# Kernel tuning notes

Measured on AMD Instinct MI355X. Metric: run time of the kernel, lower is better.

## Reference

```python
import jax, jax.numpy as jnp
import numpy as np

N, E, H, C, IN = 20000, 640000, 4, 64, 256
HC = H * C
NEG_SLOPE = 0.2


def setup_inputs() -> dict:
    key = jax.random.key(0)
    ks = jax.random.split(key, 24)
    rn = lambda k, s: jax.random.normal(k, s, jnp.float32) * 0.05
    return {
        "x": jax.random.normal(ks[0], (N, IN), jnp.float32),
        "edge_index": jax.random.randint(ks[1], (2, E), 0, N),
        "confidence": jax.random.normal(ks[2], (N,), jnp.float32),
        "w_in": rn(ks[3], (IN, C)), "b_in": jnp.zeros((C,), jnp.float32),
        "lin_w0": rn(ks[4], (C, HC)),
        "lin_w12": rn(ks[5], (2, HC, HC)),
        "att_src": rn(ks[6], (3, H, C)),
        "att_dst": rn(ks[7], (3, H, C)),
        "gat_bias": jnp.zeros((3, HC), jnp.float32),
        "conf_w": rn(ks[8], (HC, 1)), "conf_b": jnp.zeros((1,), jnp.float32),
        "nc_w1": rn(ks[9], (HC, C)), "nc_b1": jnp.zeros((C,), jnp.float32),
        "nc_w2": rn(ks[10], (C, 1)), "nc_b2": jnp.zeros((1,), jnp.float32),
        "oc_w1": rn(ks[11], (HC, C)), "oc_b1": jnp.zeros((C,), jnp.float32),
        "oc_w2": rn(ks[12], (C, 1)), "oc_b2": jnp.zeros((1,), jnp.float32),
        "ec_w1": rn(ks[13], (HC, C)), "ec_b1": jnp.zeros((C,), jnp.float32),
        "ec_w2": rn(ks[14], (C, 4)), "ec_b2": jnp.zeros((4,), jnp.float32),
    }


def _gat_layer(h_in, src, dst, n, lin_w, a_src, a_dst, bias):
    # h_in: (n, in_ch). PyG GATConv: linear -> per-edge attn -> segment softmax -> scatter-add.
    h = (h_in @ lin_w).reshape(n, H, C)
    s_src = jnp.einsum("nhc,hc->nh", h, a_src)  # (n, H)
    s_dst = jnp.einsum("nhc,hc->nh", h, a_dst)
    alpha = jax.nn.leaky_relu(s_src[src] + s_dst[dst], NEG_SLOPE)  # (E', H)
    # softmax over incoming edges of each dst node (self-loops guarantee coverage)
    amax = jax.ops.segment_max(alpha, dst, num_segments=n)
    ex = jnp.exp(alpha - amax[dst])
    denom = jax.ops.segment_sum(ex, dst, num_segments=n)
    coef = ex / jnp.maximum(denom[dst], 1e-16)
    msg = h[src] * coef[:, :, None]  # (E', H, C)
    out = jax.ops.segment_sum(msg, dst, num_segments=n)
    return out.reshape(n, HC) + bias


def reference(x, edge_index, confidence, w_in, b_in, lin_w0, lin_w12,
              att_src, att_dst, gat_bias, conf_w, conf_b,
              nc_w1, nc_b1, nc_w2, nc_b2, oc_w1, oc_b1, oc_w2, oc_b2,
              ec_w1, ec_b1, ec_w2, ec_b2):
    n = x.shape[0]
    loops = jnp.arange(n)
    src = jnp.concatenate([edge_index[0], loops])  # PyG add_self_loops=True
    dst = jnp.concatenate([edge_index[1], loops])
    h = jax.nn.relu(x @ w_in + b_in)  # input_proj + relu (dropout off in eval)
    lin_ws = [lin_w0, lin_w12[0], lin_w12[1]]
    conf_norm = jax.nn.sigmoid(confidence)  # (n,)
    for i in range(3):
        h_new = _gat_layer(h, src, dst, n, lin_ws[i], att_src[i], att_dst[i], gat_bias[i])
        cw = jax.nn.sigmoid(h_new @ conf_w + conf_b)[:, 0] * conf_norm
        h_new = h_new * cw[:, None]
        h = h + h_new if h.shape[-1] == h_new.shape[-1] else h_new
        if i < 2:
            h = jax.nn.relu(h)
    mlp = lambda w1, b1, w2, b2: jax.nn.relu(h @ w1 + b1) @ w2 + b2
    node_pred = jax.nn.sigmoid(mlp(nc_w1, nc_b1, nc_w2, nc_b2))[:, 0]
    origin_pred = jax.nn.sigmoid(mlp(oc_w1, oc_b1, oc_w2, oc_b2))[:, 0]
    error_type_pred = mlp(ec_w1, ec_b1, ec_w2, ec_b2)
    return node_pred, origin_pred, error_type_pred, h
```

## Files before the change

### kernel.cpp

```cpp
#include <hip/hip_runtime.h>
#include <cstdint>
#include <cstddef>

#define NN   20000
#define NPAD 20224
#define EE   640000
#define E2   660000
#define HHD  4
#define CC   64
#define HC   256
#define NEG  0.2f

#define NBUK 313
#define NBLK 129
#define EPB  5120
#define SCN  (NBUK * NBLK)

typedef short bf16x8 __attribute__((ext_vector_type(8)));
typedef float f32x4 __attribute__((ext_vector_type(4)));

__device__ __forceinline__ float sigmoidf_(float x) { return 1.0f / (1.0f + __expf(-x)); }

__device__ __forceinline__ float wred_sum(float v) {
#pragma unroll
    for (int d = 32; d; d >>= 1) v += __shfl_xor(v, d, 64);
    return v;
}

__device__ __forceinline__ unsigned short f2bf(float f) {
    unsigned u = __float_as_uint(f);
    u = (u + 0x7fff + ((u >> 16) & 1)) >> 16;
    return (unsigned short)u;
}
__device__ __forceinline__ float bfval(unsigned short h) { return __uint_as_float(((unsigned)h) << 16); }
__device__ __forceinline__ float bf_lo(unsigned u) { return __uint_as_float(u << 16); }
__device__ __forceinline__ float bf_hi(unsigned u) { return __uint_as_float(u & 0xffff0000u); }

__global__ __launch_bounds__(256) void hist_edges(const int* __restrict__ ei,
                                                  int* __restrict__ bhist) {
    __shared__ int h[NBUK];
    int bl = blockIdx.x, t = threadIdx.x;
    for (int i = t; i < NBUK; i += 256) h[i] = 0;
    __syncthreads();
    int e0 = bl * EPB;
#pragma unroll 4
    for (int i = t; i < EPB; i += 256) {
        int e = e0 + i;
        if (e < E2) {
            int d = (e < EE) ? ei[EE + e] : (e - EE);
            atomicAdd(&h[d >> 6], 1);
        }
    }
    __syncthreads();
    for (int i = t; i < NBUK; i += 256) bhist[i * NBLK + bl] = h[i];
}

__global__ __launch_bounds__(1024) void scan_hist(const int* __restrict__ bhist,
                                                  int* __restrict__ sbase) {
    __shared__ int buf[1024];
    int t = threadIdx.x;
    int base = t * 40;
    int local[40];
    int s = 0;
#pragma unroll
    for (int i = 0; i < 40; i++) {
        int idx = base + i;
        int v = (idx < SCN) ? bhist[idx] : 0;
        local[i] = v;
        s += v;
    }
    buf[t] = s;
    __syncthreads();
    for (int d = 1; d < 1024; d <<= 1) {
        int tv = (t >= d) ? buf[t - d] : 0;
        __syncthreads();
        buf[t] += tv;
        __syncthreads();
    }
    int run = buf[t] - s;
#pragma unroll
    for (int i = 0; i < 40; i++) {
        int idx = base + i;
        if (idx < SCN) sbase[idx] = run;
        run += local[i];
    }
}

__global__ __launch_bounds__(256) void scatter_bucket(const int* __restrict__ ei,
                                                      const int* __restrict__ sbase,
                                                      unsigned int* __restrict__ ebuf) {
    __shared__ int cur[NBUK];
    int bl = blockIdx.x, t = threadIdx.x;
    for (int i = t; i < NBUK; i += 256) cur[i] = sbase[i * NBLK + bl];
    __syncthreads();
    int e0 = bl * EPB;
#pragma unroll 4
    for (int i = t; i < EPB; i += 256) {
        int e = e0 + i;
        if (e < E2) {
            int s, d;
            if (e < EE) { s = ei[e]; d = ei[EE + e]; }
            else        { s = e - EE; d = s; }
            int p = atomicAdd(&cur[d >> 6], 1);
            ebuf[p] = ((unsigned int)(d & 63) << 15) | (unsigned int)s;
        }
    }
}

__global__ __launch_bounds__(256) void build_csr(const unsigned int* __restrict__ ebuf,
                                                 const int* __restrict__ sbase,
                                                 int* __restrict__ off,
                                                 int* __restrict__ csr) {
    __shared__ int hist[64], sc[64], curl[64];
    int bu = blockIdx.x, t = threadIdx.x;
    int base = sbase[bu * NBLK];
    int end  = (bu + 1 < NBUK) ? sbase[(bu + 1) * NBLK] : E2;
    int ne = end - base;
    if (t < 64) hist[t] = 0;
    __syncthreads();
    for (int i = t; i < ne; i += 256) {
        int dl = (int)(ebuf[base + i] >> 15);
        atomicAdd(&hist[dl], 1);
    }
    __syncthreads();
    if (t < 64) sc[t] = hist[t];
    __syncthreads();
    for (int d = 1; d < 64; d <<= 1) {
        int v = (t < 64 && t >= d) ? sc[t - d] : 0;
        __syncthreads();
        if (t < 64) sc[t] += v;
        __syncthreads();
    }
    int n0 = bu * 64;
    if (t < 64) {
        int ex = base + sc[t] - hist[t];
        if (n0 + t < NN) off[n0 + t] = ex;
        curl[t] = ex;
    }
    if (bu == NBUK - 1 && t == 0) off[NN] = E2;
    __syncthreads();
    for (int i = t; i < ne; i += 256) {
        unsigned int v = ebuf[base + i];
        int dl = (int)(v >> 15);
        int p = atomicAdd(&curl[dl], 1);
        csr[p] = (int)(v & 0x7fffu);
    }
}

#define WTOT 212992
__global__ void prep_inputs(const float* __restrict__ x,
                            const float* __restrict__ w_in, const float* __restrict__ lin_w0,
                            const float* __restrict__ lin_w12,
                            const float* __restrict__ nc1, const float* __restrict__ oc1,
                            const float* __restrict__ ec1,
                            const float* __restrict__ nb, const float* __restrict__ ob,
                            const float* __restrict__ eb,
                            unsigned short* __restrict__ whi,
                            float* __restrict__ bcat,
                            unsigned short* __restrict__ xh, unsigned short* __restrict__ xl) {
    int idx = blockIdx.x * 256 + threadIdx.x;
    if (idx < NN * 64) {
        float4 v = ((const float4*)x)[idx];
        ushort4 hi, lo;
        hi.x = f2bf(v.x); lo.x = f2bf(v.x - bfval(hi.x));
        hi.y = f2bf(v.y); lo.y = f2bf(v.y - bfval(hi.y));
        hi.z = f2bf(v.z); lo.z = f2bf(v.z - bfval(hi.z));
        hi.w = f2bf(v.w); lo.w = f2bf(v.w - bfval(hi.w));
        ((ushort4*)xh)[idx] = hi;
        ((ushort4*)xl)[idx] = lo;
    }
    if (idx < 192) {
        int g = idx >> 6, jj = idx & 63;
        const float* b = (g == 0) ? nb : ((g == 1) ? ob : eb);
        bcat[idx] = b[jj];
    }
    if (idx >= WTOT) return;
    float v;
    if (idx < 16384) {
        int n = idx >> 8, k = idx & 255;
        v = w_in[k * 64 + n];
    } else if (idx < 32768) {
        int r = idx - 16384;
        int n = r >> 6, k = r & 63;
        v = lin_w0[k * 256 + n];
    } else if (idx < 98304) {
        int r = idx - 32768;
        int n = r >> 8, k = r & 255;
        v = lin_w12[k * 256 + n];
    } else if (idx < 163840) {
        int r = idx - 98304;
        int n = r >> 8, k = r & 255;
        v = lin_w12[65536 + k * 256 + n];
    } else {
        int r = idx - 163840;
        int n = r >> 8, k = r & 255;
        int g = n >> 6, jj = n & 63;
        const float* w = (g == 0) ? nc1 : ((g == 1) ? oc1 : ec1);
        v = w[k * 64 + jj];
    }
    whi[idx] = f2bf(v);
}

template <int K, int OUT_CH, int MODE, int NT>
__global__ __launch_bounds__(256) void gemm_lds(
    const unsigned short* __restrict__ Ahp, const unsigned short* __restrict__ Alp,
    const unsigned short* __restrict__ Wh,
    const float* __restrict__ bias,
    unsigned short* __restrict__ Outh, unsigned short* __restrict__ Outl,
    const float* __restrict__ a_src, const float* __restrict__ a_dst,
    float* __restrict__ s_src, float* __restrict__ s_dst,
    const float* __restrict__ w2n, const float* __restrict__ w2o,
    const float* __restrict__ w2e,
    const float* __restrict__ b2n, const float* __restrict__ b2o,
    const float* __restrict__ b2e,
    float* __restrict__ outbuf, int nreal) {
    constexpr int LB = K + 8;
    constexpr int NS = K / 32;
    __shared__ unsigned short Bh[64 * LB];
    const int tid = threadIdx.x;
    const int wv = tid >> 6, lane = tid & 63;
    const int quad = lane >> 4, ln = lane & 15;
    const int mb = blockIdx.x * 64;
    const int r0 = mb + wv * 16 + ln;

    const unsigned short* aph = Ahp + (size_t)r0 * K + quad * 8;
    const unsigned short* apl = Alp + (size_t)r0 * K + quad * 8;
    bf16x8 ah[NS], al[NS];
#pragma unroll
    for (int s = 0; s < NS; s++) {
        ah[s] = *(const bf16x8*)(aph + s * 32);
        al[s] = *(const bf16x8*)(apl + s * 32);
    }

    for (int ct = 0; ct < NT; ct++) {
        const int cb = ct * 64;
        if (ct > 0) __syncthreads();

        constexpr int NCHK = 64 * (K / 8);
#pragma unroll
        for (int i = 0; i < NCHK / 256; i++) {
            int flat = tid + i * 256;
            int r = flat / (K / 8);
            int c = (flat % (K / 8)) * 8;
            *(uint4*)&Bh[r * LB + c] = *(const uint4*)&Wh[(size_t)(cb + r) * K + c];
        }
        __syncthreads();

        f32x4 acc[4];
#pragma unroll
        for (int j = 0; j < 4; j++) {
            acc[j][0] = 0.f; acc[j][1] = 0.f; acc[j][2] = 0.f; acc[j][3] = 0.f;
        }

#pragma unroll
        for (int s = 0; s < NS; s++) {
#pragma unroll
            for (int cg = 0; cg < 4; cg++) {
                bf16x8 bh = *(const bf16x8*)&Bh[(cg * 16 + ln) * LB + quad * 8 + s * 32];
                acc[cg] = __builtin_amdgcn_mfma_f32_16x16x32_bf16(ah[s], bh, acc[cg], 0, 0, 0);
                acc[cg] = __builtin_amdgcn_mfma_f32_16x16x32_bf16(al[s], bh, acc[cg], 0, 0, 0);
            }
        }

        if (MODE == 1) {
            float av[4], dv[4];
#pragma unroll
            for (int cg = 0; cg < 4; cg++) {
                av[cg] = a_src[cb + cg * 16 + ln];
                dv[cg] = a_dst[cb + cg * 16 + ln];
            }
#pragma unroll
            for (int reg = 0; reg < 4; reg++) {
                float ps = 0.f, pd = 0.f;
#pragma unroll
                for (int cg = 0; cg < 4; cg++) {
                    float t = acc[cg][reg];
                    ps += t * av[cg];
                    pd += t * dv[cg];
                }
#pragma unroll
                for (int d = 1; d < 16; d <<= 1) {
                    ps += __shfl_xor(ps, d, 64);
                    pd += __shfl_xor(pd, d, 64);
                }
                if (ln == 0) {
                    int row = mb + wv * 16 + quad * 4 + reg;
                    if (row < nreal) {
                        s_src[row * 4 + ct] = ps;
                        s_dst[row * 4 + ct] = pd;
                    }
                }
            }
        }

        if (MODE == 3) {
            float bv[4];
#pragma unroll
            for (int cg = 0; cg < 4; cg++) bv[cg] = bias[cb + cg * 16 + ln];
            if (ct < 2) {
                const float* w2 = (ct == 0) ? w2n : w2o;
                float b2 = (ct == 0) ? b2n[0] : b2o[0];
                float wv2[4];
#pragma unroll
                for (int cg = 0; cg < 4; cg++) wv2[cg] = w2[cg * 16 + ln];
#pragma unroll
                for (int reg = 0; reg < 4; reg++) {
                    float t = 0.f;
#pragma unroll
                    for (int cg = 0; cg < 4; cg++) {
                        float tv = fmaxf(acc[cg][reg] + bv[cg], 0.f);
                        t += tv * wv2[cg];
                    }
#pragma unroll
                    for (int d = 1; d < 16; d <<= 1) t += __shfl_xor(t, d, 64);
                    int row = mb + wv * 16 + quad * 4 + reg;
                    if (ln == 0 && row < nreal)
                        outbuf[ct * NN + row] = sigmoidf_(t + b2);
                }
            } else {
                float4 w4[4];
#pragma unroll
                for (int cg = 0; cg < 4; cg++) w4[cg] = ((const float4*)w2e)[cg * 16 + ln];
#pragma unroll
                for (int reg = 0; reg < 4; reg++) {
                    float e0 = 0.f, e1 = 0.f, e2 = 0.f, e3 = 0.f;
#pragma unroll
                    for (int cg = 0; cg < 4; cg++) {
                        float tv = fmaxf(acc[cg][reg] + bv[cg], 0.f);
                        e0 += tv * w4[cg].x; e1 += tv * w4[cg].y;
                        e2 += tv * w4[cg].z; e3 += tv * w4[cg].w;
                    }
#pragma unroll
                    for (int d = 1; d < 16; d <<= 1) {
                        e0 += __shfl_xor(e0, d, 64); e1 += __shfl_xor(e1, d, 64);
                        e2 += __shfl_xor(e2, d, 64); e3 += __shfl_xor(e3, d, 64);
                    }
                    int row = mb + wv * 16 + quad * 4 + reg;
                    if (ln == 0 && row < nreal) {
                        float4 ev = make_float4(e0 + b2e[0], e1 + b2e[1], e2 + b2e[2], e3 + b2e[3]);
                        *(float4*)&outbuf[2 * NN + row * 4] = ev;
                    }
                }
            }
            continue;
        }

#pragma unroll
        for (int cg = 0; cg < 4; cg++) {
            int col = cb + cg * 16 + ln;
            int rbase = mb + wv * 16 + quad * 4;
#pragma unroll
            for (int reg = 0; reg < 4; reg++) {
                float v = acc[cg][reg];
                int r = rbase + reg;
                if (MODE == 0) {
                    v += bias[col]; v = fmaxf(v, 0.f);
                    unsigned short hi = f2bf(v);
                    Outh[(size_t)r * OUT_CH + col] = hi;
                    Outl[(size_t)r * OUT_CH + col] = f2bf(v - bfval(hi));
                } else if (MODE == 1) {
                    Outh[(size_t)r * OUT_CH + col] = f2bf(v);
                }
            }
        }
    }
}

__global__ __launch_bounds__(256) void gat_node(const unsigned short* __restrict__ hhb,
                                                const float* __restrict__ s_src,
                                                const float* __restrict__ s_dst,
                                                const int* __restrict__ csr_src,
                                                const int* __restrict__ csr_off,
                                                const float* __restrict__ gbias,
                                                const float* __restrict__ conf_w,
                                                const float* __restrict__ conf_b,
                                                const float* __restrict__ confid,
                                                unsigned short* __restrict__ h_hi,
                                                unsigned short* __restrict__ h_lo,
                                                float* __restrict__ outbuf,
                                                int layer) {
    __shared__ float Lc[4][64];
    __shared__ int   Ls[4][16];
    int wv = threadIdx.x >> 6;
    int lane = threadIdx.x & 63;
    int n = blockIdx.x * 4 + wv;
    int myhead = lane >> 4, slot = lane & 15;
    int off0 = csr_off[n];
    int deg = csr_off[n + 1] - off0;
    const int* cp = csr_src + off0;
    const unsigned short* hrow = hhb + lane * 4;
    float sdm = s_dst[n * 4 + myhead];

    float ax = 0.f, ay = 0.f, az = 0.f, aw = 0.f, smp = 0.f;
    int nch = (deg + 15) >> 4;
    bool valid = slot < deg;
    int sl = cp[valid ? slot : deg - 1];
    float ssv = s_src[sl * 4 + myhead];
    for (int t = 0; t < nch; t++) {
        float a = ssv + sdm;
        a = a > 0.f ? a : NEG * a;
        float c = valid ? __expf(a) : 0.f;
        smp += c;
        Lc[wv][lane] = c;
        if (myhead == 0) Ls[wv][slot] = sl;
        __builtin_amdgcn_wave_barrier();
        float4 c0 = *(const float4*)&Lc[wv][myhead * 16 + 0];
        float4 c1 = *(const float4*)&Lc[wv][myhead * 16 + 4];
        float4 c2 = *(const float4*)&Lc[wv][myhead * 16 + 8];
        float4 c3 = *(const float4*)&Lc[wv][myhead * 16 + 12];
        int4 s0 = *(const int4*)&Ls[wv][0];
        int4 s1 = *(const int4*)&Ls[wv][4];
        int4 s2 = *(const int4*)&Ls[wv][8];
        int4 s3 = *(const int4*)&Ls[wv][12];
        __builtin_amdgcn_wave_barrier();
        if (t + 1 < nch) {
            int i = ((t + 1) << 4) + slot;
            valid = i < deg;
            sl = cp[valid ? i : deg - 1];
            ssv = s_src[sl * 4 + myhead];
        }
        float cf[16] = {c0.x, c0.y, c0.z, c0.w, c1.x, c1.y, c1.z, c1.w,
                        c2.x, c2.y, c2.z, c2.w, c3.x, c3.y, c3.z, c3.w};
        int sv[16] = {s0.x, s0.y, s0.z, s0.w, s1.x, s1.y, s1.z, s1.w,
                      s2.x, s2.y, s2.z, s2.w, s3.x, s3.y, s3.z, s3.w};
#pragma unroll
        for (int q = 0; q < 16; q++) {
            uint2 u = *(const uint2*)(hrow + ((size_t)sv[q] << 8));
            ax += cf[q] * bf_lo(u.x); ay += cf[q] * bf_hi(u.x);
            az += cf[q] * bf_lo(u.y); aw += cf[q] * bf_hi(u.y);
        }
    }
    smp += __shfl_xor(smp, 1, 64);
    smp += __shfl_xor(smp, 2, 64);
    smp += __shfl_xor(smp, 4, 64);
    smp += __shfl_xor(smp, 8, 64);
    float inv = 1.0f / fmaxf(smp, 1e-16f);
    ax *= inv; ay *= inv; az *= inv; aw *= inv;

    float4 b4 = *(const float4*)&gbias[lane * 4];
    float hx = ax + b4.x, hy = ay + b4.y, hz = az + b4.z, hw = aw + b4.w;
    float4 cw4 = *(const float4*)&conf_w[lane * 4];
    float local = hx * cw4.x + hy * cw4.y + hz * cw4.z + hw * cw4.w;
    float tot = wred_sum(local);
    float cw = sigmoidf_(tot + conf_b[0]) * sigmoidf_(confid[n]);
    hx *= cw; hy *= cw; hz *= cw; hw *= cw;
    if (layer > 0) {
        ushort4 ph = *(const ushort4*)&h_hi[(size_t)n * HC + lane * 4];
        ushort4 pl = *(const ushort4*)&h_lo[(size_t)n * HC + lane * 4];
        hx += bfval(ph.x) + bfval(pl.x);
        hy += bfval(ph.y) + bfval(pl.y);
        hz += bfval(ph.z) + bfval(pl.z);
        hw += bfval(ph.w) + bfval(pl.w);
    }
    if (layer < 2) {
        hx = fmaxf(hx, 0.f); hy = fmaxf(hy, 0.f);
        hz = fmaxf(hz, 0.f); hw = fmaxf(hw, 0.f);
    } else {
        *(float4*)&outbuf[6 * NN + (size_t)n * HC + lane * 4] =
            make_float4(hx, hy, hz, hw);
    }
    ushort4 oh, ol;
    oh.x = f2bf(hx); ol.x = f2bf(hx - bfval(oh.x));
    oh.y = f2bf(hy); ol.y = f2bf(hy - bfval(oh.y));
    oh.z = f2bf(hz); ol.z = f2bf(hz - bfval(oh.z));
    oh.w = f2bf(hw); ol.w = f2bf(hw - bfval(oh.w));
    *(ushort4*)&h_hi[(size_t)n * HC + lane * 4] = oh;
    *(ushort4*)&h_lo[(size_t)n * HC + lane * 4] = ol;
}

extern "C" void kernel_launch(void* const* d_in, const int* in_sizes, int n_in,
                              void* d_out, int out_size, void* d_ws, size_t ws_size,
                              hipStream_t stream) {
    const float* x       = (const float*)d_in[0];
    const int*   ei      = (const int*)d_in[1];
    const float* conf    = (const float*)d_in[2];
    const float* w_in    = (const float*)d_in[3];
    const float* b_in    = (const float*)d_in[4];
    const float* lin_w0  = (const float*)d_in[5];
    const float* lin_w12 = (const float*)d_in[6];
    const float* att_src = (const float*)d_in[7];
    const float* att_dst = (const float*)d_in[8];
    const float* gbias   = (const float*)d_in[9];
    const float* conf_w  = (const float*)d_in[10];
    const float* conf_b  = (const float*)d_in[11];
    const float* nc_w1   = (const float*)d_in[12];
    const float* nc_b1   = (const float*)d_in[13];
    const float* nc_w2   = (const float*)d_in[14];
    const float* nc_b2   = (const float*)d_in[15];
    const float* oc_w1   = (const float*)d_in[16];
    const float* oc_b1   = (const float*)d_in[17];
    const float* oc_w2   = (const float*)d_in[18];
    const float* oc_b2   = (const float*)d_in[19];
    const float* ec_w1   = (const float*)d_in[20];
    const float* ec_b1   = (const float*)d_in[21];
    const float* ec_w2   = (const float*)d_in[22];
    const float* ec_b2   = (const float*)d_in[23];
    float* out = (float*)d_out;

    char* p = (char*)d_ws;
    auto alloc = [&](size_t bytes) -> void* {
        void* r = (void*)p;
        p += (bytes + 255) & ~(size_t)255;
        return r;
    };
    unsigned short* h_hi = (unsigned short*)alloc((size_t)NPAD * HC * 2);
    unsigned short* h_lo = (unsigned short*)alloc((size_t)NPAD * HC * 2);
    unsigned short* hh   = (unsigned short*)alloc((size_t)NPAD * HC * 2);
    unsigned short* h0h  = (unsigned short*)alloc((size_t)NPAD * CC * 2);
    unsigned short* h0l  = (unsigned short*)alloc((size_t)NPAD * CC * 2);
    float*          ssrc = (float*)alloc((size_t)NN * 4 * 4);
    float*          sdst = (float*)alloc((size_t)NN * 4 * 4);
    int*            off  = (int*)alloc((size_t)(NN + 1) * 4);
    int*            csr  = (int*)alloc((size_t)E2 * 4);
    int*            bhist= (int*)alloc((size_t)SCN * 4);
    int*            sbase= (int*)alloc((size_t)SCN * 4);
    unsigned short* whi  = (unsigned short*)alloc((size_t)WTOT * 2);
    float*          bcat = (float*)alloc((size_t)192 * 4);
    unsigned short* xh   = (unsigned short*)alloc((size_t)NPAD * 256 * 2 * 2);
    unsigned short* xl   = xh + (size_t)NPAD * 256;
    unsigned int*   ebuf = (unsigned int*)xh;

    const unsigned short* wt_in = whi;
    const unsigned short* wt_l0 = whi + 16384;
    const unsigned short* wt_a  = whi + 32768;
    const unsigned short* wt_b  = whi + 98304;
    const unsigned short* wt_hd = whi + 163840;

    hist_edges<<<NBLK, 256, 0, stream>>>(ei, bhist);
    scan_hist<<<1, 1024, 0, stream>>>(bhist, sbase);
    scatter_bucket<<<NBLK, 256, 0, stream>>>(ei, sbase, ebuf);
    build_csr<<<NBUK, 256, 0, stream>>>(ebuf, sbase, off, csr);

    prep_inputs<<<(NN * 64 + 255) / 256, 256, 0, stream>>>(
        x, w_in, lin_w0, lin_w12, nc_w1, oc_w1, ec_w1, nc_b1, oc_b1, ec_b1,
        whi, bcat, xh, xl);

    gemm_lds<256, 64, 0, 1><<<dim3(NPAD / 64, 1), 256, 0, stream>>>(
        xh, xl, wt_in, b_in, h0h, h0l, nullptr, nullptr, nullptr, nullptr,
        nullptr, nullptr, nullptr, nullptr, nullptr, nullptr, nullptr, NN);

    gemm_lds<64, 256, 1, 4><<<dim3(NPAD / 64, 1), 256, 0, stream>>>(
        h0h, h0l, wt_l0, nullptr, hh, nullptr, att_src, att_dst, ssrc, sdst,
        nullptr, nullptr, nullptr, nullptr, nullptr, nullptr, nullptr, NN);
    gat_node<<<NN / 4, 256, 0, stream>>>(hh, ssrc, sdst, csr, off, gbias, conf_w, conf_b, conf,
                                         h_hi, h_lo, out, 0);

    for (int i = 1; i < 3; i++) {
        const unsigned short* wh = (i == 1) ? wt_a : wt_b;
        gemm_lds<256, 256, 1, 4><<<dim3(NPAD / 64, 1), 256, 0, stream>>>(
            h_hi, h_lo, wh, nullptr, hh, nullptr,
            att_src + i * HHD * CC, att_dst + i * HHD * CC, ssrc, sdst,
            nullptr, nullptr, nullptr, nullptr, nullptr, nullptr, nullptr, NN);
        gat_node<<<NN / 4, 256, 0, stream>>>(hh, ssrc, sdst, csr, off, gbias + i * HC,
                                             conf_w, conf_b, conf, h_hi, h_lo, out, i);
    }

    gemm_lds<256, 192, 3, 3><<<dim3(NPAD / 64, 1), 256, 0, stream>>>(
        h_hi, h_lo, wt_hd, bcat, nullptr, nullptr, nullptr, nullptr, nullptr, nullptr,
        nc_w2, oc_w2, ec_w2, nc_b2, oc_b2, ec_b2, out, NN);
}
```

Measured before the change: 386.0 us.

## Merge graph-CSR build kernels with input prep and projection GEMMs

Independent work is co-scheduled inside shared launches. Edge histogramming runs in the same grid as input/weight conversion. Bucket scatter runs alongside the input projection GEMM, and CSR build alongside the layer-0 GEMM, with blocks dispatched by block index. This cuts kernel launches and lets the irregular graph preprocessing overlap with dense work. It costs a separate ebuf allocation, since ebuf no longer aliases xh, which is now live concurrently. Shared memory is sized for the larger body, which may lower occupancy for the scatter/build blocks.

```diff
diff --git a/kernel.cpp b/kernel.cpp
--- a/kernel.cpp
+++ b/kernel.cpp
@@ -15,6 +15,8 @@
 #define NBLK 129
 #define EPB  5120
 #define SCN  (NBUK * NBLK)
+#define PREP_BLKS 5000
+#define GEMM_BLKS (NPAD / 64)
 
 typedef short bf16x8 __attribute__((ext_vector_type(8)));
 typedef float f32x4 __attribute__((ext_vector_type(4)));
@@ -36,10 +38,10 @@
 __device__ __forceinline__ float bf_lo(unsigned u) { return __uint_as_float(u << 16); }
 __device__ __forceinline__ float bf_hi(unsigned u) { return __uint_as_float(u & 0xffff0000u); }
 
-__global__ __launch_bounds__(256) void hist_edges(const int* __restrict__ ei,
-                                                  int* __restrict__ bhist) {
-    __shared__ int h[NBUK];
-    int bl = blockIdx.x, t = threadIdx.x;
+
+__device__ __forceinline__ void hist_body(int bl, const int* __restrict__ ei,
+                                          int* __restrict__ bhist, int* h ) {
+    int t = threadIdx.x;
     for (int i = t; i < NBUK; i += 256) h[i] = 0;
     __syncthreads();
     int e0 = bl * EPB;
@@ -55,42 +57,11 @@
     for (int i = t; i < NBUK; i += 256) bhist[i * NBLK + bl] = h[i];
 }
 
-__global__ __launch_bounds__(1024) void scan_hist(const int* __restrict__ bhist,
-                                                  int* __restrict__ sbase) {
-    __shared__ int buf[1024];
+__device__ __forceinline__ void scatter_body(int bl, const int* __restrict__ ei,
+                                             const int* __restrict__ sbase,
+                                             unsigned int* __restrict__ ebuf,
+                                             int* cur ) {
     int t = threadIdx.x;
-    int base = t * 40;
-    int local[40];
-    int s = 0;
-#pragma unroll
-    for (int i = 0; i < 40; i++) {
-        int idx = base + i;
-        int v = (idx < SCN) ? bhist[idx] : 0;
-        local[i] = v;
-        s += v;
-    }
-    buf[t] = s;
-    __syncthreads();
-    for (int d = 1; d < 1024; d <<= 1) {
-        int tv = (t >= d) ? buf[t - d] : 0;
-        __syncthreads();
-        buf[t] += tv;
-        __syncthreads();
-    }
-    int run = buf[t] - s;
-#pragma unroll
-    for (int i = 0; i < 40; i++) {
-        int idx = base + i;
-        if (idx < SCN) sbase[idx] = run;
-        run += local[i];
-    }
-}
-
-__global__ __launch_bounds__(256) void scatter_bucket(const int* __restrict__ ei,
-                                                      const int* __restrict__ sbase,
-                                                      unsigned int* __restrict__ ebuf) {
-    __shared__ int cur[NBUK];
-    int bl = blockIdx.x, t = threadIdx.x;
     for (int i = t; i < NBUK; i += 256) cur[i] = sbase[i * NBLK + bl];
     __syncthreads();
     int e0 = bl * EPB;
@@ -107,12 +78,13 @@
     }
 }
 
-__global__ __launch_bounds__(256) void build_csr(const unsigned int* __restrict__ ebuf,
-                                                 const int* __restrict__ sbase,
-                                                 int* __restrict__ off,
-                                                 int* __restrict__ csr) {
-    __shared__ int hist[64], sc[64], curl[64];
-    int bu = blockIdx.x, t = threadIdx.x;
+__device__ __forceinline__ void build_body(int bu, const unsigned int* __restrict__ ebuf,
+                                           const int* __restrict__ sbase,
+                                           int* __restrict__ off, int* __restrict__ csr,
+                                           int* hist ) {
+    int* sc = hist + 64;
+    int* curl = hist + 128;
+    int t = threadIdx.x;
     int base = sbase[bu * NBLK];
     int end  = (bu + 1 < NBUK) ? sbase[(bu + 1) * NBLK] : E2;
     int ne = end - base;
@@ -148,7 +120,8 @@
 }
 
 #define WTOT 212992
-__global__ void prep_inputs(const float* __restrict__ x,
+__device__ __forceinline__ void prep_body(int idx,
+                            const float* __restrict__ x,
                             const float* __restrict__ w_in, const float* __restrict__ lin_w0,
                             const float* __restrict__ lin_w12,
                             const float* __restrict__ nc1, const float* __restrict__ oc1,
@@ -158,7 +131,6 @@
                             unsigned short* __restrict__ whi,
                             float* __restrict__ bcat,
                             unsigned short* __restrict__ xh, unsigned short* __restrict__ xl) {
-    int idx = blockIdx.x * 256 + threadIdx.x;
     if (idx < NN * 64) {
         float4 v = ((const float4*)x)[idx];
         ushort4 hi, lo;
@@ -202,6 +174,262 @@
 }
 
 template <int K, int OUT_CH, int MODE, int NT>
+__device__ __forceinline__ void gemm_body(
+    unsigned short* Bh,
+    int mb,
+    const unsigned short* __restrict__ Ahp, const unsigned short* __restrict__ Alp,
+    const unsigned short* __restrict__ Wh,
+    const float* __restrict__ bias,
+    unsigned short* __restrict__ Outh,
+    const float* __restrict__ a_src, const float* __restrict__ a_dst,
+    float* __restrict__ s_src, float* __restrict__ s_dst,
+    const float* __restrict__ w2n, const float* __restrict__ w2o,
+    const float* __restrict__ w2e,
+    const float* __restrict__ b2n, const float* __restrict__ b2o,
+    const float* __restrict__ b2e,
+    unsigned short* __restrict__ Outl,
+    float* __restrict__ outbuf, int nreal) {
+    constexpr int LB = K + 8;
+    constexpr int NS = K / 32;
+    const int tid = threadIdx.x;
+    const int wv = tid >> 6, lane = tid & 63;
+    const int quad = lane >> 4, ln = lane & 15;
+    const int r0 = mb + wv * 16 + ln;
+
+    const unsigned short* aph = Ahp + (size_t)r0 * K + quad * 8;
+    const unsigned short* apl = Alp + (size_t)r0 * K + quad * 8;
+    bf16x8 ah[NS], al[NS];
+#pragma unroll
+    for (int s = 0; s < NS; s++) {
+        ah[s] = *(const bf16x8*)(aph + s * 32);
+        al[s] = *(const bf16x8*)(apl + s * 32);
+    }
+
+    for (int ct = 0; ct < NT; ct++) {
+        const int cb = ct * 64;
+        if (ct > 0) __syncthreads();
+
+        constexpr int NCHK = 64 * (K / 8);
+#pragma unroll
+        for (int i = 0; i < NCHK / 256; i++) {
+            int flat = tid + i * 256;
+            int r = flat / (K / 8);
+            int c = (flat % (K / 8)) * 8;
+            *(uint4*)&Bh[r * LB + c] = *(const uint4*)&Wh[(size_t)(cb + r) * K + c];
+        }
+        __syncthreads();
+
+        f32x4 acc[4];
+#pragma unroll
+        for (int j = 0; j < 4; j++) {
+            acc[j][0] = 0.f; acc[j][1] = 0.f; acc[j][2] = 0.f; acc[j][3] = 0.f;
+        }
+
+#pragma unroll
+        for (int s = 0; s < NS; s++) {
+#pragma unroll
+            for (int cg = 0; cg < 4; cg++) {
+                bf16x8 bh = *(const bf16x8*)&Bh[(cg * 16 + ln) * LB + quad * 8 + s * 32];
+                acc[cg] = __builtin_amdgcn_mfma_f32_16x16x32_bf16(ah[s], bh, acc[cg], 0, 0, 0);
+                acc[cg] = __builtin_amdgcn_mfma_f32_16x16x32_bf16(al[s], bh, acc[cg], 0, 0, 0);
+            }
+        }
+
+        if (MODE == 1) {
+            float av[4], dv[4];
+#pragma unroll
+            for (int cg = 0; cg < 4; cg++) {
+                av[cg] = a_src[cb + cg * 16 + ln];
+                dv[cg] = a_dst[cb + cg * 16 + ln];
+            }
+#pragma unroll
+            for (int reg = 0; reg < 4; reg++) {
+                float ps = 0.f, pd = 0.f;
+#pragma unroll
+                for (int cg = 0; cg < 4; cg++) {
+                    float t = acc[cg][reg];
+                    ps += t * av[cg];
+                    pd += t * dv[cg];
+                }
+#pragma unroll
+                for (int d = 1; d < 16; d <<= 1) {
+                    ps += __shfl_xor(ps, d, 64);
+                    pd += __shfl_xor(pd, d, 64);
+                }
+                if (ln == 0) {
+                    int row = mb + wv * 16 + quad * 4 + reg;
+                    if (row < nreal) {
+                        s_src[row * 4 + ct] = ps;
+                        s_dst[row * 4 + ct] = pd;
+                    }
+                }
+            }
+        }
+
+        if (MODE == 3) {
+            float bv[4];
+#pragma unroll
+            for (int cg = 0; cg < 4; cg++) bv[cg] = bias[cb + cg * 16 + ln];
+            if (ct < 2) {
+                const float* w2 = (ct == 0) ? w2n : w2o;
+                float b2 = (ct == 0) ? b2n[0] : b2o[0];
+                float wv2[4];
+#pragma unroll
+                for (int cg = 0; cg < 4; cg++) wv2[cg] = w2[cg * 16 + ln];
+#pragma unroll
+                for (int reg = 0; reg < 4; reg++) {
+                    float t = 0.f;
+#pragma unroll
+                    for (int cg = 0; cg < 4; cg++) {
+                        float tv = fmaxf(acc[cg][reg] + bv[cg], 0.f);
+                        t += tv * wv2[cg];
+                    }
+#pragma unroll
+                    for (int d = 1; d < 16; d <<= 1) t += __shfl_xor(t, d, 64);
+                    int row = mb + wv * 16 + quad * 4 + reg;
+                    if (ln == 0 && row < nreal)
+                        outbuf[ct * NN + row] = sigmoidf_(t + b2);
+                }
+            } else {
+                float4 w4[4];
+#pragma unroll
+                for (int cg = 0; cg < 4; cg++) w4[cg] = ((const float4*)w2e)[cg * 16 + ln];
+#pragma unroll
+                for (int reg = 0; reg < 4; reg++) {
+                    float e0 = 0.f, e1 = 0.f, e2 = 0.f, e3 = 0.f;
+#pragma unroll
+                    for (int cg = 0; cg < 4; cg++) {
+                        float tv = fmaxf(acc[cg][reg] + bv[cg], 0.f);
+                        e0 += tv * w4[cg].x; e1 += tv * w4[cg].y;
+                        e2 += tv * w4[cg].z; e3 += tv * w4[cg].w;
+                    }
+#pragma unroll
+                    for (int d = 1; d < 16; d <<= 1) {
+                        e0 += __shfl_xor(e0, d, 64); e1 += __shfl_xor(e1, d, 64);
+                        e2 += __shfl_xor(e2, d, 64); e3 += __shfl_xor(e3, d, 64);
+                    }
+                    int row = mb + wv * 16 + quad * 4 + reg;
+                    if (ln == 0 && row < nreal) {
+                        float4 ev = make_float4(e0 + b2e[0], e1 + b2e[1], e2 + b2e[2], e3 + b2e[3]);
+                        *(float4*)&outbuf[2 * NN + row * 4] = ev;
+                    }
+                }
+            }
+            continue;
+        }
+
+#pragma unroll
+        for (int cg = 0; cg < 4; cg++) {
+            int col = cb + cg * 16 + ln;
+            int rbase = mb + wv * 16 + quad * 4;
+#pragma unroll
+            for (int reg = 0; reg < 4; reg++) {
+                float v = acc[cg][reg];
+                int r = rbase + reg;
+                if (MODE == 0) {
+                    v += bias[col]; v = fmaxf(v, 0.f);
+                    unsigned short hi = f2bf(v);
+                    Outh[(size_t)r * OUT_CH + col] = hi;
+                    Outl[(size_t)r * OUT_CH + col] = f2bf(v - bfval(hi));
+                } else if (MODE == 1) {
+                    Outh[(size_t)r * OUT_CH + col] = f2bf(v);
+                }
+            }
+        }
+    }
+}
+
+
+__global__ __launch_bounds__(256) void prep_hist(
+    const float* __restrict__ x,
+    const float* __restrict__ w_in, const float* __restrict__ lin_w0,
+    const float* __restrict__ lin_w12,
+    const float* __restrict__ nc1, const float* __restrict__ oc1,
+    const float* __restrict__ ec1,
+    const float* __restrict__ nb, const float* __restrict__ ob,
+    const float* __restrict__ eb,
+    unsigned short* __restrict__ whi, float* __restrict__ bcat,
+    unsigned short* __restrict__ xh, unsigned short* __restrict__ xl,
+    const int* __restrict__ ei, int* __restrict__ bhist) {
+    __shared__ int h[NBUK];
+    if (blockIdx.x < PREP_BLKS) {
+        prep_body(blockIdx.x * 256 + threadIdx.x, x, w_in, lin_w0, lin_w12,
+                  nc1, oc1, ec1, nb, ob, eb, whi, bcat, xh, xl);
+    } else {
+        hist_body(blockIdx.x - PREP_BLKS, ei, bhist, h);
+    }
+}
+
+__global__ __launch_bounds__(1024) void scan_hist(const int* __restrict__ bhist,
+                                                  int* __restrict__ sbase) {
+    __shared__ int buf[1024];
+    int t = threadIdx.x;
+    int base = t * 40;
+    int local[40];
+    int s = 0;
+#pragma unroll
+    for (int i = 0; i < 40; i++) {
+        int idx = base + i;
+        int v = (idx < SCN) ? bhist[idx] : 0;
+        local[i] = v;
+        s += v;
+    }
+    buf[t] = s;
+    __syncthreads();
+    for (int d = 1; d < 1024; d <<= 1) {
+        int tv = (t >= d) ? buf[t - d] : 0;
+        __syncthreads();
+        buf[t] += tv;
+        __syncthreads();
+    }
+    int run = buf[t] - s;
+#pragma unroll
+    for (int i = 0; i < 40; i++) {
+        int idx = base + i;
+        if (idx < SCN) sbase[idx] = run;
+        run += local[i];
+    }
+}
+
+__global__ __launch_bounds__(256) void scatter_proj(
+    const int* __restrict__ ei, const int* __restrict__ sbase,
+    unsigned int* __restrict__ ebuf,
+    const unsigned short* __restrict__ xh, const unsigned short* __restrict__ xl,
+    const unsigned short* __restrict__ wt_in, const float* __restrict__ b_in,
+    unsigned short* __restrict__ h0h, unsigned short* __restrict__ h0l) {
+    __shared__ unsigned short smem[64 * (256 + 8)];
+    if (blockIdx.x < NBLK) {
+        scatter_body(blockIdx.x, ei, sbase, ebuf, (int*)smem);
+    } else {
+        gemm_body<256, 64, 0, 1>(smem, (int)(blockIdx.x - NBLK) * 64,
+                                 xh, xl, wt_in, b_in, h0h,
+                                 nullptr, nullptr, nullptr, nullptr,
+                                 nullptr, nullptr, nullptr, nullptr, nullptr, nullptr,
+                                 h0l, nullptr, NN);
+    }
+}
+
+__global__ __launch_bounds__(256) void build_l0(
+    const unsigned int* __restrict__ ebuf, const int* __restrict__ sbase,
+    int* __restrict__ off, int* __restrict__ csr,
+    const unsigned short* __restrict__ h0h, const unsigned short* __restrict__ h0l,
+    const unsigned short* __restrict__ wt_l0,
+    unsigned short* __restrict__ hh,
+    const float* __restrict__ a_src, const float* __restrict__ a_dst,
+    float* __restrict__ ssrc, float* __restrict__ sdst) {
+    __shared__ unsigned short smem[64 * (64 + 8)];
+    if (blockIdx.x < NBUK) {
+        build_body(blockIdx.x, ebuf, sbase, off, csr, (int*)smem);
+    } else {
+        gemm_body<64, 256, 1, 4>(smem, (int)(blockIdx.x - NBUK) * 64,
+                                 h0h, h0l, wt_l0, nullptr, hh,
+                                 a_src, a_dst, ssrc, sdst,
+                                 nullptr, nullptr, nullptr, nullptr, nullptr, nullptr,
+                                 nullptr, nullptr, NN);
+    }
+}
+
+template <int K, int OUT_CH, int MODE, int NT>
 __global__ __launch_bounds__(256) void gemm_lds(
     const unsigned short* __restrict__ Ahp, const unsigned short* __restrict__ Alp,
     const unsigned short* __restrict__ Wh,
@@ -214,156 +442,10 @@
     const float* __restrict__ b2n, const float* __restrict__ b2o,
     const float* __restrict__ b2e,
     float* __restrict__ outbuf, int nreal) {
-    constexpr int LB = K + 8;
-    constexpr int NS = K / 32;
-    __shared__ unsigned short Bh[64 * LB];
-    const int tid = threadIdx.x;
-    const int wv = tid >> 6, lane = tid & 63;
-    const int quad = lane >> 4, ln = lane & 15;
-    const int mb = blockIdx.x * 64;
-    const int r0 = mb + wv * 16 + ln;
-
-    const unsigned short* aph = Ahp + (size_t)r0 * K + quad * 8;
-    const unsigned short* apl = Alp + (size_t)r0 * K + quad * 8;
-    bf16x8 ah[NS], al[NS];
-#pragma unroll
-    for (int s = 0; s < NS; s++) {
-        ah[s] = *(const bf16x8*)(aph + s * 32);
-        al[s] = *(const bf16x8*)(apl + s * 32);
-    }
-
-    for (int ct = 0; ct < NT; ct++) {
-        const int cb = ct * 64;
-        if (ct > 0) __syncthreads();
-
-        constexpr int NCHK = 64 * (K / 8);
-#pragma unroll
-        for (int i = 0; i < NCHK / 256; i++) {
-            int flat = tid + i * 256;
-            int r = flat / (K / 8);
-            int c = (flat % (K / 8)) * 8;
-            *(uint4*)&Bh[r * LB + c] = *(const uint4*)&Wh[(size_t)(cb + r) * K + c];
-        }
-        __syncthreads();
-
-        f32x4 acc[4];
-#pragma unroll
-        for (int j = 0; j < 4; j++) {
-            acc[j][0] = 0.f; acc[j][1] = 0.f; acc[j][2] = 0.f; acc[j][3] = 0.f;
-        }
-
-#pragma unroll
-        for (int s = 0; s < NS; s++) {
-#pragma unroll
-            for (int cg = 0; cg < 4; cg++) {
-                bf16x8 bh = *(const bf16x8*)&Bh[(cg * 16 + ln) * LB + quad * 8 + s * 32];
-                acc[cg] = __builtin_amdgcn_mfma_f32_16x16x32_bf16(ah[s], bh, acc[cg], 0, 0, 0);
-                acc[cg] = __builtin_amdgcn_mfma_f32_16x16x32_bf16(al[s], bh, acc[cg], 0, 0, 0);
-            }
-        }
-
-        if (MODE == 1) {
-            float av[4], dv[4];
-#pragma unroll
-            for (int cg = 0; cg < 4; cg++) {
-                av[cg] = a_src[cb + cg * 16 + ln];
-                dv[cg] = a_dst[cb + cg * 16 + ln];
-            }
-#pragma unroll
-            for (int reg = 0; reg < 4; reg++) {
-                float ps = 0.f, pd = 0.f;
-#pragma unroll
-                for (int cg = 0; cg < 4; cg++) {
-                    float t = acc[cg][reg];
-                    ps += t * av[cg];
-                    pd += t * dv[cg];
-                }
-#pragma unroll
-                for (int d = 1; d < 16; d <<= 1) {
-                    ps += __shfl_xor(ps, d, 64);
-                    pd += __shfl_xor(pd, d, 64);
-                }
-                if (ln == 0) {
-                    int row = mb + wv * 16 + quad * 4 + reg;
-                    if (row < nreal) {
-                        s_src[row * 4 + ct] = ps;
-                        s_dst[row * 4 + ct] = pd;
-                    }
-                }
-            }
-        }
-
-        if (MODE == 3) {
-            float bv[4];
-#pragma unroll
-            for (int cg = 0; cg < 4; cg++) bv[cg] = bias[cb + cg * 16 + ln];
-            if (ct < 2) {
-                const float* w2 = (ct == 0) ? w2n : w2o;
-                float b2 = (ct == 0) ? b2n[0] : b2o[0];
-                float wv2[4];
-#pragma unroll
-                for (int cg = 0; cg < 4; cg++) wv2[cg] = w2[cg * 16 + ln];
-#pragma unroll
-                for (int reg = 0; reg < 4; reg++) {
-                    float t = 0.f;
-#pragma unroll
-                    for (int cg = 0; cg < 4; cg++) {
-                        float tv = fmaxf(acc[cg][reg] + bv[cg], 0.f);
-                        t += tv * wv2[cg];
-                    }
-#pragma unroll
-                    for (int d = 1; d < 16; d <<= 1) t += __shfl_xor(t, d, 64);
-                    int row = mb + wv * 16 + quad * 4 + reg;
-                    if (ln == 0 && row < nreal)
-                        outbuf[ct * NN + row] = sigmoidf_(t + b2);
-                }
-            } else {
-                float4 w4[4];
-#pragma unroll
-                for (int cg = 0; cg < 4; cg++) w4[cg] = ((const float4*)w2e)[cg * 16 + ln];
-#pragma unroll
-                for (int reg = 0; reg < 4; reg++) {
-                    float e0 = 0.f, e1 = 0.f, e2 = 0.f, e3 = 0.f;
-#pragma unroll
-                    for (int cg = 0; cg < 4; cg++) {
-                        float tv = fmaxf(acc[cg][reg] + bv[cg], 0.f);
-                        e0 += tv * w4[cg].x; e1 += tv * w4[cg].y;
-                        e2 += tv * w4[cg].z; e3 += tv * w4[cg].w;
-                    }
-#pragma unroll
-                    for (int d = 1; d < 16; d <<= 1) {
-                        e0 += __shfl_xor(e0, d, 64); e1 += __shfl_xor(e1, d, 64);
-                        e2 += __shfl_xor(e2, d, 64); e3 += __shfl_xor(e3, d, 64);
-                    }
-                    int row = mb + wv * 16 + quad * 4 + reg;
-                    if (ln == 0 && row < nreal) {
-                        float4 ev = make_float4(e0 + b2e[0], e1 + b2e[1], e2 + b2e[2], e3 + b2e[3]);
-                        *(float4*)&outbuf[2 * NN + row * 4] = ev;
-                    }
-                }
-            }
-            continue;
-        }
-
-#pragma unroll
-        for (int cg = 0; cg < 4; cg++) {
-            int col = cb + cg * 16 + ln;
-            int rbase = mb + wv * 16 + quad * 4;
-#pragma unroll
-            for (int reg = 0; reg < 4; reg++) {
-                float v = acc[cg][reg];
-                int r = rbase + reg;
-                if (MODE == 0) {
-                    v += bias[col]; v = fmaxf(v, 0.f);
-                    unsigned short hi = f2bf(v);
-                    Outh[(size_t)r * OUT_CH + col] = hi;
-                    Outl[(size_t)r * OUT_CH + col] = f2bf(v - bfval(hi));
-                } else if (MODE == 1) {
-                    Outh[(size_t)r * OUT_CH + col] = f2bf(v);
-                }
-            }
-        }
-    }
+    __shared__ unsigned short Bh[64 * (K + 8)];
+    gemm_body<K, OUT_CH, MODE, NT>(Bh, blockIdx.x * 64, Ahp, Alp, Wh, bias, Outh,
+                                   a_src, a_dst, s_src, s_dst,
+                                   w2n, w2o, w2e, b2n, b2o, b2e, Outl, outbuf, nreal);
 }
 
 __global__ __launch_bounds__(256) void gat_node(const unsigned short* __restrict__ hhb,
@@ -514,11 +596,11 @@
     int*            csr  = (int*)alloc((size_t)E2 * 4);
     int*            bhist= (int*)alloc((size_t)SCN * 4);
     int*            sbase= (int*)alloc((size_t)SCN * 4);
+    unsigned int*   ebuf = (unsigned int*)alloc((size_t)E2 * 4);
     unsigned short* whi  = (unsigned short*)alloc((size_t)WTOT * 2);
     float*          bcat = (float*)alloc((size_t)192 * 4);
     unsigned short* xh   = (unsigned short*)alloc((size_t)NPAD * 256 * 2 * 2);
     unsigned short* xl   = xh + (size_t)NPAD * 256;
-    unsigned int*   ebuf = (unsigned int*)xh;
 
     const unsigned short* wt_in = whi;
     const unsigned short* wt_l0 = whi + 16384;
@@ -526,28 +608,24 @@
     const unsigned short* wt_b  = whi + 98304;
     const unsigned short* wt_hd = whi + 163840;
 
-    hist_edges<<<NBLK, 256, 0, stream>>>(ei, bhist);
+    prep_hist<<<PREP_BLKS + NBLK, 256, 0, stream>>>(
+        x, w_in, lin_w0, lin_w12, nc_w1, oc_w1, ec_w1, nc_b1, oc_b1, ec_b1,
+        whi, bcat, xh, xl, ei, bhist);
+
     scan_hist<<<1, 1024, 0, stream>>>(bhist, sbase);
-    scatter_bucket<<<NBLK, 256, 0, stream>>>(ei, sbase, ebuf);
-    build_csr<<<NBUK, 256, 0, stream>>>(ebuf, sbase, off, csr);
-
-    prep_inputs<<<(NN * 64 + 255) / 256, 256, 0, stream>>>(
-        x, w_in, lin_w0, lin_w12, nc_w1, oc_w1, ec_w1, nc_b1, oc_b1, ec_b1,
-        whi, bcat, xh, xl);
-
-    gemm_lds<256, 64, 0, 1><<<dim3(NPAD / 64, 1), 256, 0, stream>>>(
-        xh, xl, wt_in, b_in, h0h, h0l, nullptr, nullptr, nullptr, nullptr,
-        nullptr, nullptr, nullptr, nullptr, nullptr, nullptr, nullptr, NN);
-
-    gemm_lds<64, 256, 1, 4><<<dim3(NPAD / 64, 1), 256, 0, stream>>>(
-        h0h, h0l, wt_l0, nullptr, hh, nullptr, att_src, att_dst, ssrc, sdst,
-        nullptr, nullptr, nullptr, nullptr, nullptr, nullptr, nullptr, NN);
+
+    scatter_proj<<<NBLK + GEMM_BLKS, 256, 0, stream>>>(
+        ei, sbase, ebuf, xh, xl, wt_in, b_in, h0h, h0l);
+
+    build_l0<<<NBUK + GEMM_BLKS, 256, 0, stream>>>(
+        ebuf, sbase, off, csr, h0h, h0l, wt_l0, hh, att_src, att_dst, ssrc, sdst);
+
     gat_node<<<NN / 4, 256, 0, stream>>>(hh, ssrc, sdst, csr, off, gbias, conf_w, conf_b, conf,
                                          h_hi, h_lo, out, 0);
 
     for (int i = 1; i < 3; i++) {
         const unsigned short* wh = (i == 1) ? wt_a : wt_b;
-        gemm_lds<256, 256, 1, 4><<<dim3(NPAD / 64, 1), 256, 0, stream>>>(
+        gemm_lds<256, 256, 1, 4><<<dim3(GEMM_BLKS, 1), 256, 0, stream>>>(
             h_hi, h_lo, wh, nullptr, hh, nullptr,
             att_src + i * HHD * CC, att_dst + i * HHD * CC, ssrc, sdst,
             nullptr, nullptr, nullptr, nullptr, nullptr, nullptr, nullptr, NN);
@@ -555,7 +633,7 @@
                                              conf_w, conf_b, conf, h_hi, h_lo, out, i);
     }
 
-    gemm_lds<256, 192, 3, 3><<<dim3(NPAD / 64, 1), 256, 0, stream>>>(
+    gemm_lds<256, 192, 3, 3><<<dim3(GEMM_BLKS, 1), 256, 0, stream>>>(
         h_hi, h_lo, wt_hd, bcat, nullptr, nullptr, nullptr, nullptr, nullptr, nullptr,
         nc_w2, oc_w2, ec_w2, nc_b2, oc_b2, ec_b2, out, NN);
 }
```

After: 370.8 us (median of 3 runs). 3.9% less time.
